# Optimization experiments

Measured on AMD Instinct MI355X. Metric: run time of the kernel, lower is better.

The kernel has to match this reference:

```python
import jax, jax.numpy as jnp
import numpy as np

HID = 128
HEADS = 4
CH = HID // HEADS          # 32
EDGE_DIM = 2 * HID         # H_update mode
GROUPS = 8
NEG_SLOPE = 0.2
EPS_GN = 1e-5
EPS_LN = 1e-5
N_NODES = 32768
N_EDGES = 524288


def setup_inputs() -> dict:
    key = jax.random.key(0)
    ks = jax.random.split(key, 32)
    N, E, C = N_NODES, N_EDGES, HID
    s = lambda fan: 1.0 / np.sqrt(fan)
    inp = dict(
        h_target=jax.random.normal(ks[0], (N, C), jnp.float32),
        h_source=jax.random.normal(ks[1], (N, C), jnp.float32),
        pos=jax.random.normal(ks[2], (N, 2), jnp.float32),
        t_emb=jax.random.normal(ks[3], (N, C), jnp.float32),
        edge_index=jax.random.randint(ks[4], (2, E), 0, N, jnp.int32),
        # AdaGN params
        gn_gamma=jnp.ones((C,), jnp.float32),
        gn_beta=jnp.zeros((C,), jnp.float32),
        fc_W=jax.random.normal(ks[5], (C, 2 * C), jnp.float32) * s(C),
        fc_b=jnp.zeros((2 * C,), jnp.float32),
        # GATv2 params
        Wl=jax.random.normal(ks[6], (C, HEADS * CH), jnp.float32) * s(C),
        bl=jnp.zeros((HEADS * CH,), jnp.float32),
        Wr=jax.random.normal(ks[7], (C, HEADS * CH), jnp.float32) * s(C),
        br=jnp.zeros((HEADS * CH,), jnp.float32),
        We=jax.random.normal(ks[8], (EDGE_DIM, HEADS * CH), jnp.float32) * s(EDGE_DIM),
        att=jax.random.normal(ks[9], (HEADS, CH), jnp.float32) * s(CH),
        gat_bias=jnp.zeros((HEADS * CH,), jnp.float32),
        # post GAT linear
        Wpost=jax.random.normal(ks[10], (C, C), jnp.float32) * s(C),
        bpost=jnp.zeros((C,), jnp.float32),
        # update MLP: LayerNorm -> Linear -> GELU -> Linear
        ln_g=jnp.ones((C,), jnp.float32),
        ln_b=jnp.zeros((C,), jnp.float32),
        W1=jax.random.normal(ks[11], (C, C), jnp.float32) * s(C),
        b1=jnp.zeros((C,), jnp.float32),
        W2=jax.random.normal(ks[12], (C, C), jnp.float32) * s(C),
        b2=jnp.zeros((C,), jnp.float32),
    )
    return inp


def _adagn(x, cond, gn_gamma, gn_beta, fc_W, fc_b):
    N, C = x.shape
    xg = x.reshape(N, GROUPS, C // GROUPS)
    mu = xg.mean(-1, keepdims=True)
    var = xg.var(-1, keepdims=True)
    normed = ((xg - mu) * jax.lax.rsqrt(var + EPS_GN)).reshape(N, C)
    normed = normed * gn_gamma + gn_beta
    style = cond @ fc_W + fc_b
    gamma, beta = jnp.split(style, 2, axis=-1)
    return normed * (1.0 + gamma) + beta


def reference(h_target, h_source, pos, t_emb, edge_index,
              gn_gamma, gn_beta, fc_W, fc_b,
              Wl, bl, Wr, br, We, att, gat_bias,
              Wpost, bpost, ln_g, ln_b, W1, b1, W2, b2):
    N, C = h_source.shape
    src, dst = edge_index[0], edge_index[1]

    h_src_mod = _adagn(h_source, t_emb, gn_gamma, gn_beta, fc_W, fc_b)

    # physics edge features (H_update mode)
    d_vec = pos[src] - pos[dst]                       # [E,2]
    dx, dy = d_vec[:, 0:1], d_vec[:, 1:2]
    dist_sq = jnp.maximum((d_vec ** 2).sum(-1, keepdims=True), 1e-8)
    grad_mag = (h_src_mod[src] - h_src_mod[dst]) / dist_sq   # [E,C]
    edge_attr = jnp.concatenate([grad_mag * (-dy), grad_mag * dx], axis=-1)  # [E,2C]

    # GATv2Conv (eval mode, no dropout)
    xl = (h_src_mod @ Wl + bl).reshape(N, HEADS, CH)  # source transform
    xr = (h_src_mod @ Wr + br).reshape(N, HEADS, CH)  # target transform
    e = (edge_attr @ We).reshape(-1, HEADS, CH)
    z = jax.nn.leaky_relu(xl[src] + xr[dst] + e, NEG_SLOPE)   # [E,H,Ch]
    logit = jnp.einsum('ehc,hc->eh', z, att)                  # [E,H]
    m = jax.ops.segment_max(logit, dst, num_segments=N)       # [N,H]
    m = jnp.where(jnp.isfinite(m), m, 0.0)
    ex = jnp.exp(logit - m[dst])
    denom = jax.ops.segment_sum(ex, dst, num_segments=N)      # [N,H]
    alpha = ex / (denom[dst] + 1e-16)                         # [E,H]
    msg = xl[src] * alpha[..., None]                          # [E,H,Ch]
    aggr = jax.ops.segment_sum(msg, dst, num_segments=N).reshape(N, HEADS * CH)
    aggr = aggr + gat_bias

    aggr = aggr @ Wpost + bpost

    # update MLP with residual
    mu = aggr.mean(-1, keepdims=True)
    var = aggr.var(-1, keepdims=True)
    ln = (aggr - mu) * jax.lax.rsqrt(var + EPS_LN) * ln_g + ln_b
    h = jax.nn.gelu(ln @ W1 + b1, approximate=False) @ W2 + b2
    return h_target + h
```

## Files before the change

### kernel.cpp

```cpp
#include <hip/hip_runtime.h>
#include <hip/hip_bf16.h>
#include <math.h>

#define HID 128

typedef __bf16 bf16x8 __attribute__((ext_vector_type(8)));
typedef float f32x4 __attribute__((ext_vector_type(4)));
typedef float nf4 __attribute__((ext_vector_type(4)));
union BF8 { uint4 u; bf16x8 v; unsigned short s[8]; };

__device__ __forceinline__ unsigned short f2bf(float x) {
  unsigned u = __float_as_uint(x);
  unsigned r = u + 0x7FFFu + ((u >> 16) & 1u);
  return (unsigned short)(r >> 16);
}
__device__ __forceinline__ float bf2f(unsigned short h) {
  return __uint_as_float(((unsigned)h) << 16);
}
__device__ __forceinline__ void ld2bf(const unsigned short* p, float& x, float& y) {
  unsigned v = *(const unsigned*)p;
  x = __uint_as_float((v & 0xFFFFu) << 16);
  y = __uint_as_float(v & 0xFFFF0000u);
}
__device__ __forceinline__ float2 pk_add2(float2 a, float2 b) {
  return make_float2(a.x + b.x, a.y + b.y);
}
__device__ __forceinline__ float2 pk_sub2(float2 a, float2 b) {
  return make_float2(a.x - b.x, a.y - b.y);
}
__device__ __forceinline__ float2 pk_fma2(float2 a, float2 b, float2 c) {
  return make_float2(fmaf(a.x, b.x, c.x), fmaf(a.y, b.y, c.y));
}
__device__ __forceinline__ float2 pk_max2(float2 a, float2 b) {
  return make_float2(fmaxf(a.x, b.x), fmaxf(a.y, b.y));
}
__device__ __forceinline__ float2 pk_muls2(float2 a, float b) {
  return make_float2(a.x * b, a.y * b);
}

__global__ __launch_bounds__(256) void k1_prep_hist(
    const float* __restrict__ fc_W, const float* __restrict__ Wl,
    const float* __restrict__ Wr, const float* __restrict__ We,
    const float* __restrict__ Wpost, const float* __restrict__ W1,
    const float* __restrict__ W2, const float* __restrict__ bl,
    const float* __restrict__ br, const float* __restrict__ gat_bias,
    const float* __restrict__ bpost,
    unsigned short* __restrict__ fcTh, unsigned short* __restrict__ fcTl,
    unsigned short* __restrict__ WnTh, unsigned short* __restrict__ WnTl,
    unsigned short* __restrict__ WpT, unsigned short* __restrict__ W1T,
    unsigned short* __restrict__ W2T,
    float* __restrict__ bxy, float* __restrict__ bpost2,
    const int* __restrict__ edst, int* __restrict__ count, int E) {
  int bid = blockIdx.x;
  if (bid >= 578) {
    int e = (bid - 578) * 256 + threadIdx.x;
    if (e < E) atomicAdd(&count[edst[e]], 1);
    return;
  }
  int gid = bid * 256 + threadIdx.x;
  if (gid < 32768) {
    int n = gid >> 7, k = gid & 127;
    float x = fc_W[k * 256 + n];
    unsigned short h = f2bf(x);
    fcTh[n * 128 + k] = h;
    fcTl[n * 128 + k] = f2bf(x - bf2f(h));
  } else if (gid < 98304) {
    int i = gid - 32768; int n = i >> 7, k = i & 127;
    float x;
    if (n < 128)      x = Wl[k * 128 + n];
    else if (n < 256) x = Wr[k * 128 + (n - 128)];
    else if (n < 384) x = We[k * 128 + (n - 256)];
    else              x = We[(128 + k) * 128 + (n - 384)];
    unsigned short h = f2bf(x);
    WnTh[n * 128 + k] = h;
    if (n >= 256) WnTl[(n - 256) * 128 + k] = f2bf(x - bf2f(h));
  } else if (gid < 147456) {
    int i = gid - 98304; int which = i >> 14; int j = i & 16383;
    int n = j >> 7, k = j & 127;
    const float* W = (which == 0) ? Wpost : (which == 1) ? W1 : W2;
    unsigned short* T = (which == 0) ? WpT : (which == 1) ? W1T : W2T;
    T[n * 128 + k] = f2bf(W[k * 128 + n]);
  } else if (gid < 147712) {
    int j = gid - 147456;
    bxy[j] = (j < 128) ? bl[j] : br[j - 128];
  } else if (gid < 147840) {
    int t = gid - 147712;
    float s = bpost[t];
    for (int k = 0; k < 128; ++k) s += gat_bias[k] * Wpost[k * 128 + t];
    bpost2[t] = s;
  }
}

__global__ __launch_bounds__(256) void k2_style_scan(
    const float* __restrict__ A, const unsigned short* __restrict__ WTh,
    const unsigned short* __restrict__ WTl, const float* __restrict__ bias,
    float* __restrict__ C,
    const int* __restrict__ count, int* __restrict__ rowptr,
    int* __restrict__ cursor, int N, int E) {
  if (blockIdx.x == 512) {
    __shared__ int wtot[4];
    int t = threadIdx.x, lane = t & 63, wv = t >> 6;
    const int4* c4 = (const int4*)count;
    int base = t * 32;
    int s = 0;
    for (int i = 0; i < 32; ++i) {
      int4 c = c4[base + i];
      s += c.x + c.y + c.z + c.w;
    }
    int incl = s;
#pragma unroll
    for (int off = 1; off < 64; off <<= 1) {
      int v = __shfl_up(incl, off);
      if (lane >= off) incl += v;
    }
    if (lane == 63) wtot[wv] = incl;
    __syncthreads();
    if (t == 0) {
      int a0 = wtot[0], a1 = wtot[1], a2 = wtot[2];
      wtot[0] = 0; wtot[1] = a0; wtot[2] = a0 + a1; wtot[3] = a0 + a1 + a2;
    }
    __syncthreads();
    int run = wtot[wv] + incl - s;
    for (int i = 0; i < 32; ++i) {
      int4 c = c4[base + i];
      int4 r;
      r.x = run; run += c.x;
      r.y = run; run += c.y;
      r.z = run; run += c.z;
      r.w = run; run += c.w;
      ((int4*)rowptr)[base + i] = r;
      ((int4*)cursor)[base + i] = r;
    }
    if (t == 255) rowptr[N] = E;
    return;
  }
  int tid = threadIdx.x;
  int wave = tid >> 6, lane = tid & 63;
  int m = lane & 15, q = lane >> 4;
  int r0 = blockIdx.x * 64 + wave * 16;
  const float* arow = A + (size_t)(r0 + m) * 128 + q * 8;
  BF8 Ah[4], Al[4];
#pragma unroll
  for (int kc = 0; kc < 4; ++kc) {
    float4 x0 = *(const float4*)(arow + kc * 32);
    float4 x1 = *(const float4*)(arow + kc * 32 + 4);
    float xs[8] = {x0.x, x0.y, x0.z, x0.w, x1.x, x1.y, x1.z, x1.w};
#pragma unroll
    for (int j = 0; j < 8; ++j) {
      unsigned short h = f2bf(xs[j]);
      Ah[kc].s[j] = h;
      Al[kc].s[j] = f2bf(xs[j] - bf2f(h));
    }
  }
  for (int nt = 0; nt < 16; ++nt) {
    const unsigned short* wr  = WTh + (size_t)(nt * 16 + m) * 128 + q * 8;
    const unsigned short* wrl = WTl + (size_t)(nt * 16 + m) * 128 + q * 8;
    f32x4 acc = {0.f, 0.f, 0.f, 0.f};
#pragma unroll
    for (int kc = 0; kc < 4; ++kc) {
      BF8 bh, blo;
      bh.u  = *(const uint4*)(wr + kc * 32);
      blo.u = *(const uint4*)(wrl + kc * 32);
      acc = __builtin_amdgcn_mfma_f32_16x16x32_bf16(Ah[kc].v, bh.v, acc, 0, 0, 0);
      acc = __builtin_amdgcn_mfma_f32_16x16x32_bf16(Al[kc].v, bh.v, acc, 0, 0, 0);
      acc = __builtin_amdgcn_mfma_f32_16x16x32_bf16(Ah[kc].v, blo.v, acc, 0, 0, 0);
    }
    int n = nt * 16 + m;
    float bv = bias[n];
#pragma unroll
    for (int i = 0; i < 4; ++i) {
      int row = r0 + q * 4 + i;
      C[(size_t)row * 256 + n] = acc[i] + bv;
    }
  }
}

__global__ __launch_bounds__(256) void k3_node_scatter(
    const float* __restrict__ h_source, const float* __restrict__ style,
    const float* __restrict__ gn_gamma, const float* __restrict__ gn_beta,
    const unsigned short* __restrict__ WnTh, const unsigned short* __restrict__ WnTl,
    const float* __restrict__ bxy,
    unsigned short* __restrict__ packed, unsigned short* __restrict__ xrArr,
    const int* __restrict__ esrc, const int* __restrict__ edst,
    const float* __restrict__ pos, int* __restrict__ cursor,
    nf4* __restrict__ meta, int E) {
  int bid = blockIdx.x;
  if (bid >= 256) {
    int e = (bid - 256) * 256 + threadIdx.x;
    if (e >= E) return;
    int src = esrc[e], dst = edst[e];
    int p = atomicAdd(&cursor[dst], 1);
    float2 ps = *(const float2*)(pos + 2 * src);
    float2 pd = *(const float2*)(pos + 2 * dst);
    float dx = ps.x - pd.x, dy = ps.y - pd.y;
    float d2 = fmaxf(dx * dx + dy * dy, 1e-8f);
    nf4 v = {__int_as_float(src), -dy / d2, dx / d2, 0.0f};
    meta[p] = v;
    return;
  }
  int tid = threadIdx.x, wave = tid >> 6, lane = tid & 63;
  int m = lane & 15, q = lane >> 4;
  int r0 = bid * 128 + wave * 32;
  BF8 Ah[2][4], Al[2][4];
#pragma unroll
  for (int set = 0; set < 2; ++set) {
    int r = r0 + set * 16 + m;
    const float* hrow = h_source + (size_t)r * 128;
    const float* srow = style + (size_t)r * 256;
#pragma unroll
    for (int kc = 0; kc < 4; ++kc) {
      int ch = q * 8 + kc * 32;
      float4 x0 = *(const float4*)(hrow + ch);
      float4 x1 = *(const float4*)(hrow + ch + 4);
      float xs[8] = {x0.x, x0.y, x0.z, x0.w, x1.x, x1.y, x1.z, x1.w};
      float s8 = 0.f, q8 = 0.f;
#pragma unroll
      for (int j = 0; j < 8; ++j) { s8 += xs[j]; q8 += xs[j] * xs[j]; }
      float s16 = s8 + __shfl_xor(s8, 16);
      float q16 = q8 + __shfl_xor(q8, 16);
      float mu = s16 * (1.0f / 16.0f);
      float var = q16 * (1.0f / 16.0f) - mu * mu;
      float rv = rsqrtf(var + 1e-5f);
      float4 g0 = *(const float4*)(gn_gamma + ch);
      float4 g1 = *(const float4*)(gn_gamma + ch + 4);
      float4 be0 = *(const float4*)(gn_beta + ch);
      float4 be1 = *(const float4*)(gn_beta + ch + 4);
      float4 sg0 = *(const float4*)(srow + ch);
      float4 sg1 = *(const float4*)(srow + ch + 4);
      float4 sb0 = *(const float4*)(srow + 128 + ch);
      float4 sb1 = *(const float4*)(srow + 128 + ch + 4);
      float gg[8] = {g0.x, g0.y, g0.z, g0.w, g1.x, g1.y, g1.z, g1.w};
      float bb[8] = {be0.x, be0.y, be0.z, be0.w, be1.x, be1.y, be1.z, be1.w};
      float sg[8] = {sg0.x, sg0.y, sg0.z, sg0.w, sg1.x, sg1.y, sg1.z, sg1.w};
      float sb[8] = {sb0.x, sb0.y, sb0.z, sb0.w, sb1.x, sb1.y, sb1.z, sb1.w};
#pragma unroll
      for (int j = 0; j < 8; ++j) {
        float v = ((xs[j] - mu) * rv * gg[j] + bb[j]) * (1.0f + sg[j]) + sb[j];
        unsigned short h = f2bf(v);
        Ah[set][kc].s[j] = h;
        Al[set][kc].s[j] = f2bf(v - bf2f(h));
      }
    }
  }
  for (int nt = 0; nt < 32; ++nt) {
    f32x4 acc0 = {0.f, 0.f, 0.f, 0.f};
    f32x4 acc1 = {0.f, 0.f, 0.f, 0.f};
    const unsigned short* wr = WnTh + (size_t)(nt * 16 + m) * 128 + q * 8;
    if (nt < 16) {
#pragma unroll
      for (int kc = 0; kc < 4; ++kc) {
        BF8 bh; bh.u = *(const uint4*)(wr + kc * 32);
        acc0 = __builtin_amdgcn_mfma_f32_16x16x32_bf16(Ah[0][kc].v, bh.v, acc0, 0, 0, 0);
        acc1 = __builtin_amdgcn_mfma_f32_16x16x32_bf16(Ah[1][kc].v, bh.v, acc1, 0, 0, 0);
      }
    } else {
      const unsigned short* wl = WnTl + (size_t)((nt - 16) * 16 + m) * 128 + q * 8;
#pragma unroll
      for (int kc = 0; kc < 4; ++kc) {
        BF8 bh, blo;
        bh.u  = *(const uint4*)(wr + kc * 32);
        blo.u = *(const uint4*)(wl + kc * 32);
        acc0 = __builtin_amdgcn_mfma_f32_16x16x32_bf16(Ah[0][kc].v, bh.v, acc0, 0, 0, 0);
        acc0 = __builtin_amdgcn_mfma_f32_16x16x32_bf16(Al[0][kc].v, bh.v, acc0, 0, 0, 0);
        acc0 = __builtin_amdgcn_mfma_f32_16x16x32_bf16(Ah[0][kc].v, blo.v, acc0, 0, 0, 0);
        acc1 = __builtin_amdgcn_mfma_f32_16x16x32_bf16(Ah[1][kc].v, bh.v, acc1, 0, 0, 0);
        acc1 = __builtin_amdgcn_mfma_f32_16x16x32_bf16(Al[1][kc].v, bh.v, acc1, 0, 0, 0);
        acc1 = __builtin_amdgcn_mfma_f32_16x16x32_bf16(Ah[1][kc].v, blo.v, acc1, 0, 0, 0);
      }
    }
    int n = nt * 16 + m;
    float bv = (nt < 16) ? bxy[n] : 0.0f;
#pragma unroll
    for (int set = 0; set < 2; ++set) {
      f32x4 a = set ? acc1 : acc0;
#pragma unroll
      for (int i = 0; i < 4; ++i) {
        int row = r0 + set * 16 + q * 4 + i;
        unsigned short h = f2bf(a[i] + bv);
        if (nt < 8)       packed[(size_t)row * 384 + n] = h;
        else if (nt < 16) xrArr[(size_t)row * 128 + (n - 128)] = h;
        else              packed[(size_t)row * 384 + 128 + (n - 256)] = h;
      }
    }
  }
}

__device__ __forceinline__ void edge_step(nf4 mt, const unsigned* __restrict__ packedW,
                                          int lane, float2 xr, float2 Ad, float2 Bd,
                                          float a0, float a1,
                                          float& m, float& l, float2& s) {
  int si = __float_as_int(mt.x);
  const unsigned* pr = packedW + (size_t)si * 192;
  unsigned wxl = pr[lane];
  unsigned wA  = pr[64 + lane];
  unsigned wB  = pr[128 + lane];
  float2 xl = make_float2(__uint_as_float(wxl << 16), __uint_as_float(wxl & 0xFFFF0000u));
  float2 A  = make_float2(__uint_as_float(wA << 16),  __uint_as_float(wA & 0xFFFF0000u));
  float2 B  = make_float2(__uint_as_float(wB << 16),  __uint_as_float(wB & 0xFFFF0000u));
  float2 z = pk_add2(xl, xr);
  z = pk_fma2(make_float2(mt.y, mt.y), pk_sub2(A, Ad), z);
  z = pk_fma2(make_float2(mt.z, mt.z), pk_sub2(B, Bd), z);
  float2 zl = pk_max2(z, pk_muls2(z, 0.2f));
  float p = fmaf(a0, zl.x, a1 * zl.y);
#pragma unroll
  for (int mm = 8; mm >= 1; mm >>= 1) p += __shfl_xor(p, mm);
  if (p <= m) {
    float ex = expf(p - m);
    l += ex;
    s = pk_fma2(make_float2(ex, ex), xl, s);
  } else {
    float sc = expf(m - p);
    l = fmaf(l, sc, 1.0f);
    s = pk_fma2(make_float2(sc, sc), s, xl);
    m = p;
  }
}

__global__ __launch_bounds__(256) void k_edge(const int* __restrict__ rowptr,
                                              const nf4* __restrict__ meta,
                                              const unsigned short* __restrict__ packed,
                                              const unsigned short* __restrict__ xrArr,
                                              const float* __restrict__ att,
                                              float* __restrict__ aggr, int N) {
  int tid = threadIdx.x;
  int d = blockIdx.x * 4 + (tid >> 6);
  if (d >= N) return;
  int lane = tid & 63;
  int c0 = lane * 2;
  float2 av = *(const float2*)(att + c0);
  const unsigned* packedW = (const unsigned*)packed;
  float2 xr, Ad, Bd;
  ld2bf(xrArr + (size_t)d * 128 + c0, xr.x, xr.y);
  {
    const unsigned* pd = packedW + (size_t)d * 192;
    unsigned wA = pd[64 + lane], wB = pd[128 + lane];
    Ad = make_float2(__uint_as_float(wA << 16), __uint_as_float(wA & 0xFFFF0000u));
    Bd = make_float2(__uint_as_float(wB << 16), __uint_as_float(wB & 0xFFFF0000u));
  }
  int beg = rowptr[d], end = rowptr[d + 1];
  float m1 = -INFINITY, l1 = 0.f; float2 s1 = make_float2(0.f, 0.f);
  float m2 = -INFINITY, l2 = 0.f; float2 s2 = make_float2(0.f, 0.f);
  int j = beg;
  if (j + 1 < end) {
    nf4 mt0 = meta[j], mt1 = meta[j + 1];
    for (; j + 3 < end; j += 2) {
      nf4 nx0 = meta[j + 2], nx1 = meta[j + 3];
      edge_step(mt0, packedW, lane, xr, Ad, Bd, av.x, av.y, m1, l1, s1);
      edge_step(mt1, packedW, lane, xr, Ad, Bd, av.x, av.y, m2, l2, s2);
      mt0 = nx0; mt1 = nx1;
    }
    edge_step(mt0, packedW, lane, xr, Ad, Bd, av.x, av.y, m1, l1, s1);
    edge_step(mt1, packedW, lane, xr, Ad, Bd, av.x, av.y, m2, l2, s2);
    j += 2;
  }
  if (j < end) {
    nf4 mt = meta[j];
    edge_step(mt, packedW, lane, xr, Ad, Bd, av.x, av.y, m1, l1, s1);
  }
  float nm = fmaxf(m1, m2);
  float sc1 = (m1 == nm) ? 1.0f : expf(m1 - nm);
  float sc2 = (m2 == nm) ? 1.0f : expf(m2 - nm);
  float l = fmaf(l1, sc1, l2 * sc2);
  float o0 = fmaf(s1.x, sc1, s2.x * sc2);
  float o1 = fmaf(s1.y, sc1, s2.y * sc2);
  float inv = 1.0f / (l + 1e-16f);
  *(float2*)&aggr[(size_t)d * 128 + c0] = make_float2(o0 * inv, o1 * inv);
}

__global__ __launch_bounds__(256) void k_mlp(const float* __restrict__ aggr,
                                             const unsigned short* __restrict__ WpT,
                                             const unsigned short* __restrict__ W1T,
                                             const unsigned short* __restrict__ W2T,
                                             const float* __restrict__ bpost2,
                                             const float* __restrict__ b1,
                                             const float* __restrict__ b2,
                                             const float* __restrict__ ln_g,
                                             const float* __restrict__ ln_b,
                                             const float* __restrict__ h_target,
                                             float* __restrict__ out) {
  __shared__ unsigned short Tb[64 * 136];
  __shared__ unsigned short Ub[64 * 136];
  int tid = threadIdx.x, wave = tid >> 6, lane = tid & 63;
  int m = lane & 15, q = lane >> 4;
  int r0 = blockIdx.x * 64 + wave * 16;
  int rb0 = wave * 16;
  BF8 Af[4];
  {
    const float* arow = aggr + (size_t)(r0 + m) * 128 + q * 8;
#pragma unroll
    for (int kc = 0; kc < 4; ++kc) {
      float4 x0 = *(const float4*)(arow + kc * 32);
      float4 x1 = *(const float4*)(arow + kc * 32 + 4);
      float xs[8] = {x0.x, x0.y, x0.z, x0.w, x1.x, x1.y, x1.z, x1.w};
#pragma unroll
      for (int jj = 0; jj < 8; ++jj) Af[kc].s[jj] = f2bf(xs[jj]);
    }
  }
  f32x4 acc[8];
#pragma unroll
  for (int t = 0; t < 8; ++t) {
    const unsigned short* wr = WpT + (size_t)(t * 16 + m) * 128 + q * 8;
    f32x4 a = {0.f, 0.f, 0.f, 0.f};
#pragma unroll
    for (int kc = 0; kc < 4; ++kc) {
      BF8 bh; bh.u = *(const uint4*)(wr + kc * 32);
      a = __builtin_amdgcn_mfma_f32_16x16x32_bf16(Af[kc].v, bh.v, a, 0, 0, 0);
    }
    acc[t] = a;
  }
  float sum[4] = {0, 0, 0, 0}, sq[4] = {0, 0, 0, 0};
#pragma unroll
  for (int t = 0; t < 8; ++t) {
    float bv = bpost2[t * 16 + m];
#pragma unroll
    for (int i = 0; i < 4; ++i) {
      float v = acc[t][i] + bv;
      acc[t][i] = v;
      sum[i] += v;
      sq[i] += v * v;
    }
  }
#pragma unroll
  for (int i = 0; i < 4; ++i) {
#pragma unroll
    for (int w = 1; w <= 8; w <<= 1) {
      sum[i] += __shfl_xor(sum[i], w);
      sq[i] += __shfl_xor(sq[i], w);
    }
  }
  float mu[4], rv[4];
#pragma unroll
  for (int i = 0; i < 4; ++i) {
    mu[i] = sum[i] * (1.0f / 128.0f);
    float var = sq[i] * (1.0f / 128.0f) - mu[i] * mu[i];
    rv[i] = rsqrtf(var + 1e-5f);
  }
#pragma unroll
  for (int t = 0; t < 8; ++t) {
    int n = t * 16 + m;
    float g = ln_g[n], b = ln_b[n];
#pragma unroll
    for (int i = 0; i < 4; ++i) {
      float v = (acc[t][i] - mu[i]) * rv[i] * g + b;
      Tb[(rb0 + q * 4 + i) * 136 + n] = f2bf(v);
    }
  }
  __syncthreads();
  BF8 Bf[4];
  {
    const unsigned short* tp = Tb + (rb0 + m) * 136 + q * 8;
#pragma unroll
    for (int kc = 0; kc < 4; ++kc) Bf[kc].u = *(const uint4*)(tp + kc * 32);
  }
#pragma unroll
  for (int t = 0; t < 8; ++t) {
    const unsigned short* wr = W1T + (size_t)(t * 16 + m) * 128 + q * 8;
    f32x4 a = {0.f, 0.f, 0.f, 0.f};
#pragma unroll
    for (int kc = 0; kc < 4; ++kc) {
      BF8 bh; bh.u = *(const uint4*)(wr + kc * 32);
      a = __builtin_amdgcn_mfma_f32_16x16x32_bf16(Bf[kc].v, bh.v, a, 0, 0, 0);
    }
    acc[t] = a;
  }
#pragma unroll
  for (int t = 0; t < 8; ++t) {
    int n = t * 16 + m;
    float bv = b1[n];
#pragma unroll
    for (int i = 0; i < 4; ++i) {
      float v = acc[t][i] + bv;
      v = 0.5f * v * (1.0f + erff(v * 0.70710678118654752f));
      Ub[(rb0 + q * 4 + i) * 136 + n] = f2bf(v);
    }
  }
  __syncthreads();
  BF8 Cf[4];
  {
    const unsigned short* up = Ub + (rb0 + m) * 136 + q * 8;
#pragma unroll
    for (int kc = 0; kc < 4; ++kc) Cf[kc].u = *(const uint4*)(up + kc * 32);
  }
#pragma unroll
  for (int t = 0; t < 8; ++t) {
    const unsigned short* wr = W2T + (size_t)(t * 16 + m) * 128 + q * 8;
    f32x4 a = {0.f, 0.f, 0.f, 0.f};
#pragma unroll
    for (int kc = 0; kc < 4; ++kc) {
      BF8 bh; bh.u = *(const uint4*)(wr + kc * 32);
      a = __builtin_amdgcn_mfma_f32_16x16x32_bf16(Cf[kc].v, bh.v, a, 0, 0, 0);
    }
    int n = t * 16 + m;
    float bv = b2[n];
#pragma unroll
    for (int i = 0; i < 4; ++i) {
      size_t off = (size_t)(r0 + q * 4 + i) * 128 + n;
      out[off] = a[i] + bv + h_target[off];
    }
  }
}

extern "C" void kernel_launch(void* const* d_in, const int* in_sizes, int n_in,
                              void* d_out, int out_size, void* d_ws, size_t ws_size,
                              hipStream_t stream) {
  const float* h_target = (const float*)d_in[0];
  const float* h_source = (const float*)d_in[1];
  const float* pos      = (const float*)d_in[2];
  const float* t_emb    = (const float*)d_in[3];
  const int*   eidx     = (const int*)d_in[4];
  const float* gn_gamma = (const float*)d_in[5];
  const float* gn_beta  = (const float*)d_in[6];
  const float* fc_W     = (const float*)d_in[7];
  const float* fc_b     = (const float*)d_in[8];
  const float* Wl       = (const float*)d_in[9];
  const float* bl       = (const float*)d_in[10];
  const float* Wr       = (const float*)d_in[11];
  const float* br       = (const float*)d_in[12];
  const float* We       = (const float*)d_in[13];
  const float* att      = (const float*)d_in[14];
  const float* gat_bias = (const float*)d_in[15];
  const float* Wpost    = (const float*)d_in[16];
  const float* bpost    = (const float*)d_in[17];
  const float* ln_g     = (const float*)d_in[18];
  const float* ln_b     = (const float*)d_in[19];
  const float* W1       = (const float*)d_in[20];
  const float* b1       = (const float*)d_in[21];
  const float* W2       = (const float*)d_in[22];
  const float* b2       = (const float*)d_in[23];

  const int N = in_sizes[0] / HID;
  const int E = in_sizes[4] / 2;
  const int* esrc = eidx;
  const int* edst = eidx + E;

  float* ws = (float*)d_ws;
  const size_t MF = 1024 * 1024;
  float* style  = ws;
  float* aggr   = ws;
  unsigned short* packed = (unsigned short*)(ws + 8 * MF);
  unsigned short* xrArr  = (unsigned short*)(ws + 14 * MF);
  nf4*   meta   = (nf4*)(ws + 16 * MF);
  int*   rowptr = (int*)(ws + 18 * MF);
  int*   count  = rowptr + 32832;
  int*   cursor = count + 32832;
  unsigned short* wgt = (unsigned short*)(ws + 18 * MF + 131072);
  unsigned short* fcTh = wgt;
  unsigned short* fcTl = wgt + 32768;
  unsigned short* WnTh = wgt + 65536;
  unsigned short* WnTl = wgt + 131072;
  unsigned short* WpT  = wgt + 163840;
  unsigned short* W1T  = wgt + 180224;
  unsigned short* W2T  = wgt + 196608;
  float* bxy    = (float*)(wgt + 212992);
  float* bpost2 = bxy + 256;
  const size_t needed = (size_t)(18 * MF + 131072 + 106496 + 512) * 4;
  if (ws_size < needed) return;

  dim3 blk(256);
  const int histB = (E + 255) / 256;

  (void)hipMemsetAsync(count, 0, (size_t)N * 4, stream);
  k1_prep_hist<<<578 + histB, blk, 0, stream>>>(
      fc_W, Wl, Wr, We, Wpost, W1, W2, bl, br, gat_bias, bpost,
      fcTh, fcTl, WnTh, WnTl, WpT, W1T, W2T, bxy, bpost2, edst, count, E);
  k2_style_scan<<<513, blk, 0, stream>>>(t_emb, fcTh, fcTl, fc_b, style,
                                         count, rowptr, cursor, N, E);
  k3_node_scatter<<<256 + histB, blk, 0, stream>>>(
      h_source, style, gn_gamma, gn_beta, WnTh, WnTl, bxy, packed, xrArr,
      esrc, edst, pos, cursor, meta, E);
  k_edge<<<(N + 3) / 4, blk, 0, stream>>>(rowptr, meta, packed, xrArr, att, aggr, N);
  k_mlp<<<N / 64, blk, 0, stream>>>(aggr, WpT, W1T, W2T, bpost2, b1, b2, ln_g, ln_b,
                                    h_target, (float*)d_out);
}
```

Measured before the change: 364.5 us.

## Interleave per-node edge features and software-pipeline gathers in the GAT edge kernel

Reorders the packed per-node buffer so each lane's xl, A and B bf16 pairs sit next to each other, so one 12-byte load per lane replaces three separate 4-byte gathers per edge. The edge loop now prefetches the gathered rows one iteration ahead to overlap gather latency with compute. It also replaces the shuffle reduction with DPP moves, uses fast __expf, and uses a lazy max-rescale threshold (+8) to skip most rescale branches. The threshold and fast exp slightly change numerics. The longer prefetch chain raises register pressure.

```diff
diff --git a/kernel.cpp b/kernel.cpp
--- a/kernel.cpp
+++ b/kernel.cpp
@@ -7,7 +7,10 @@
 typedef __bf16 bf16x8 __attribute__((ext_vector_type(8)));
 typedef float f32x4 __attribute__((ext_vector_type(4)));
 typedef float nf4 __attribute__((ext_vector_type(4)));
+typedef float v2f __attribute__((ext_vector_type(2)));
 union BF8 { uint4 u; bf16x8 v; unsigned short s[8]; };
+
+struct __attribute__((packed, aligned(4))) U3 { unsigned a, b, c; };
 
 __device__ __forceinline__ unsigned short f2bf(float x) {
   unsigned u = __float_as_uint(x);
@@ -22,20 +25,11 @@
   x = __uint_as_float((v & 0xFFFFu) << 16);
   y = __uint_as_float(v & 0xFFFF0000u);
 }
-__device__ __forceinline__ float2 pk_add2(float2 a, float2 b) {
-  return make_float2(a.x + b.x, a.y + b.y);
-}
-__device__ __forceinline__ float2 pk_sub2(float2 a, float2 b) {
-  return make_float2(a.x - b.x, a.y - b.y);
-}
-__device__ __forceinline__ float2 pk_fma2(float2 a, float2 b, float2 c) {
-  return make_float2(fmaf(a.x, b.x, c.x), fmaf(a.y, b.y, c.y));
-}
-__device__ __forceinline__ float2 pk_max2(float2 a, float2 b) {
-  return make_float2(fmaxf(a.x, b.x), fmaxf(a.y, b.y));
-}
-__device__ __forceinline__ float2 pk_muls2(float2 a, float b) {
-  return make_float2(a.x * b, a.y * b);
+__device__ __forceinline__ v2f bfpair(unsigned w) {
+  v2f r;
+  r.x = __uint_as_float(w << 16);
+  r.y = __uint_as_float(w & 0xFFFF0000u);
+  return r;
 }
 
 __global__ __launch_bounds__(256) void k1_prep_hist(
@@ -270,6 +264,16 @@
     }
     int n = nt * 16 + m;
     float bv = (nt < 16) ? bxy[n] : 0.0f;
+    int pidx;
+    if (nt < 8) {
+      pidx = 6 * (n >> 1) + (n & 1);
+    } else if (nt >= 16) {
+      int t = n - 256;
+      int c = t & 127;
+      pidx = 6 * (c >> 1) + ((t < 128) ? 2 : 4) + (c & 1);
+    } else {
+      pidx = -1;
+    }
 #pragma unroll
     for (int set = 0; set < 2; ++set) {
       f32x4 a = set ? acc1 : acc0;
@@ -277,41 +281,41 @@
       for (int i = 0; i < 4; ++i) {
         int row = r0 + set * 16 + q * 4 + i;
         unsigned short h = f2bf(a[i] + bv);
-        if (nt < 8)       packed[(size_t)row * 384 + n] = h;
-        else if (nt < 16) xrArr[(size_t)row * 128 + (n - 128)] = h;
-        else              packed[(size_t)row * 384 + 128 + (n - 256)] = h;
+        if (pidx >= 0) packed[(size_t)row * 384 + pidx] = h;
+        else           xrArr[(size_t)row * 128 + (n - 128)] = h;
       }
     }
   }
 }
 
-__device__ __forceinline__ void edge_step(nf4 mt, const unsigned* __restrict__ packedW,
-                                          int lane, float2 xr, float2 Ad, float2 Bd,
-                                          float a0, float a1,
-                                          float& m, float& l, float2& s) {
-  int si = __float_as_int(mt.x);
-  const unsigned* pr = packedW + (size_t)si * 192;
-  unsigned wxl = pr[lane];
-  unsigned wA  = pr[64 + lane];
-  unsigned wB  = pr[128 + lane];
-  float2 xl = make_float2(__uint_as_float(wxl << 16), __uint_as_float(wxl & 0xFFFF0000u));
-  float2 A  = make_float2(__uint_as_float(wA << 16),  __uint_as_float(wA & 0xFFFF0000u));
-  float2 B  = make_float2(__uint_as_float(wB << 16),  __uint_as_float(wB & 0xFFFF0000u));
-  float2 z = pk_add2(xl, xr);
-  z = pk_fma2(make_float2(mt.y, mt.y), pk_sub2(A, Ad), z);
-  z = pk_fma2(make_float2(mt.z, mt.z), pk_sub2(B, Bd), z);
-  float2 zl = pk_max2(z, pk_muls2(z, 0.2f));
-  float p = fmaf(a0, zl.x, a1 * zl.y);
-#pragma unroll
-  for (int mm = 8; mm >= 1; mm >>= 1) p += __shfl_xor(p, mm);
-  if (p <= m) {
-    float ex = expf(p - m);
+__device__ __forceinline__ float dpp_red16(float p) {
+  p += __int_as_float(__builtin_amdgcn_mov_dpp(__float_as_int(p), 0xB1, 0xF, 0xF, true));
+  p += __int_as_float(__builtin_amdgcn_mov_dpp(__float_as_int(p), 0x4E, 0xF, 0xF, true));
+  p += __int_as_float(__builtin_amdgcn_mov_dpp(__float_as_int(p), 0x141, 0xF, 0xF, true));
+  p += __int_as_float(__builtin_amdgcn_mov_dpp(__float_as_int(p), 0x140, 0xF, 0xF, true));
+  return p;
+}
+
+__device__ __forceinline__ void edge_compute(nf4 mt, U3 r, v2f xr, v2f Ad, v2f Bd,
+                                             float a0, float a1,
+                                             float& m, float& l, v2f& s) {
+  v2f xl = bfpair(r.a);
+  v2f A  = bfpair(r.b);
+  v2f B  = bfpair(r.c);
+  v2f z = xl + xr;
+  z = (A - Ad) * mt.y + z;
+  z = (B - Bd) * mt.z + z;
+  v2f zq = z * 0.2f;
+  float p = fmaf(a0, fmaxf(z.x, zq.x), a1 * fmaxf(z.y, zq.y));
+  p = dpp_red16(p);
+  if (__builtin_expect(p <= m + 8.0f, 1)) {
+    float ex = __expf(p - m);
     l += ex;
-    s = pk_fma2(make_float2(ex, ex), xl, s);
+    s = xl * ex + s;
   } else {
-    float sc = expf(m - p);
+    float sc = __expf(m - p);
     l = fmaf(l, sc, 1.0f);
-    s = pk_fma2(make_float2(sc, sc), s, xl);
+    s = s * sc + xl;
     m = p;
   }
 }
@@ -327,44 +331,67 @@
   if (d >= N) return;
   int lane = tid & 63;
   int c0 = lane * 2;
+  unsigned lane12 = (unsigned)lane * 12u;
   float2 av = *(const float2*)(att + c0);
-  const unsigned* packedW = (const unsigned*)packed;
-  float2 xr, Ad, Bd;
-  ld2bf(xrArr + (size_t)d * 128 + c0, xr.x, xr.y);
-  {
-    const unsigned* pd = packedW + (size_t)d * 192;
-    unsigned wA = pd[64 + lane], wB = pd[128 + lane];
-    Ad = make_float2(__uint_as_float(wA << 16), __uint_as_float(wA & 0xFFFF0000u));
-    Bd = make_float2(__uint_as_float(wB << 16), __uint_as_float(wB & 0xFFFF0000u));
-  }
+  const char* rbase = (const char*)packed;
+  v2f xr;
+  { float x, y; ld2bf(xrArr + (size_t)d * 128 + c0, x, y); xr.x = x; xr.y = y; }
+  U3 rd = *(const U3*)(rbase + (unsigned)d * 768u + lane12);
+  v2f Ad = bfpair(rd.b), Bd = bfpair(rd.c);
   int beg = rowptr[d], end = rowptr[d + 1];
-  float m1 = -INFINITY, l1 = 0.f; float2 s1 = make_float2(0.f, 0.f);
-  float m2 = -INFINITY, l2 = 0.f; float2 s2 = make_float2(0.f, 0.f);
-  int j = beg;
-  if (j + 1 < end) {
-    nf4 mt0 = meta[j], mt1 = meta[j + 1];
-    for (; j + 3 < end; j += 2) {
-      nf4 nx0 = meta[j + 2], nx1 = meta[j + 3];
-      edge_step(mt0, packedW, lane, xr, Ad, Bd, av.x, av.y, m1, l1, s1);
-      edge_step(mt1, packedW, lane, xr, Ad, Bd, av.x, av.y, m2, l2, s2);
-      mt0 = nx0; mt1 = nx1;
-    }
-    edge_step(mt0, packedW, lane, xr, Ad, Bd, av.x, av.y, m1, l1, s1);
-    edge_step(mt1, packedW, lane, xr, Ad, Bd, av.x, av.y, m2, l2, s2);
-    j += 2;
-  }
-  if (j < end) {
+  float m1 = -INFINITY, l1 = 0.f; v2f s1 = {0.f, 0.f};
+  float m2 = -INFINITY, l2 = 0.f; v2f s2 = {0.f, 0.f};
+  int j = beg, rem = end - beg;
+  nf4 ma0 = {}, ma1 = {}, mb0 = {}, mb1 = {};
+  U3 ra0 = {}, ra1 = {};
+  if (rem >= 2) {
+    ma0 = meta[j]; ma1 = meta[j + 1];
+    ra0 = *(const U3*)(rbase + (unsigned)__float_as_int(ma0.x) * 768u + lane12);
+    ra1 = *(const U3*)(rbase + (unsigned)__float_as_int(ma1.x) * 768u + lane12);
+    if (rem >= 4) { mb0 = meta[j + 2]; mb1 = meta[j + 3]; }
+  }
+  for (; j + 5 < end; j += 2) {
+    nf4 mc0 = meta[j + 4], mc1 = meta[j + 5];
+    U3 rb0 = *(const U3*)(rbase + (unsigned)__float_as_int(mb0.x) * 768u + lane12);
+    U3 rb1 = *(const U3*)(rbase + (unsigned)__float_as_int(mb1.x) * 768u + lane12);
+    edge_compute(ma0, ra0, xr, Ad, Bd, av.x, av.y, m1, l1, s1);
+    edge_compute(ma1, ra1, xr, Ad, Bd, av.x, av.y, m2, l2, s2);
+    ma0 = mb0; ma1 = mb1; mb0 = mc0; mb1 = mc1;
+    ra0 = rb0; ra1 = rb1;
+  }
+  rem = end - j;
+  if (rem >= 4) {
+    U3 rb0 = *(const U3*)(rbase + (unsigned)__float_as_int(mb0.x) * 768u + lane12);
+    U3 rb1 = *(const U3*)(rbase + (unsigned)__float_as_int(mb1.x) * 768u + lane12);
+    edge_compute(ma0, ra0, xr, Ad, Bd, av.x, av.y, m1, l1, s1);
+    edge_compute(ma1, ra1, xr, Ad, Bd, av.x, av.y, m2, l2, s2);
+    edge_compute(mb0, rb0, xr, Ad, Bd, av.x, av.y, m1, l1, s1);
+    edge_compute(mb1, rb1, xr, Ad, Bd, av.x, av.y, m2, l2, s2);
+    if (rem == 5) {
+      nf4 mt = meta[j + 4];
+      U3 r = *(const U3*)(rbase + (unsigned)__float_as_int(mt.x) * 768u + lane12);
+      edge_compute(mt, r, xr, Ad, Bd, av.x, av.y, m1, l1, s1);
+    }
+  } else if (rem >= 2) {
+    edge_compute(ma0, ra0, xr, Ad, Bd, av.x, av.y, m1, l1, s1);
+    edge_compute(ma1, ra1, xr, Ad, Bd, av.x, av.y, m2, l2, s2);
+    if (rem == 3) {
+      nf4 mt = meta[j + 2];
+      U3 r = *(const U3*)(rbase + (unsigned)__float_as_int(mt.x) * 768u + lane12);
+      edge_compute(mt, r, xr, Ad, Bd, av.x, av.y, m1, l1, s1);
+    }
+  } else if (rem == 1) {
     nf4 mt = meta[j];
-    edge_step(mt, packedW, lane, xr, Ad, Bd, av.x, av.y, m1, l1, s1);
+    U3 r = *(const U3*)(rbase + (unsigned)__float_as_int(mt.x) * 768u + lane12);
+    edge_compute(mt, r, xr, Ad, Bd, av.x, av.y, m1, l1, s1);
   }
   float nm = fmaxf(m1, m2);
-  float sc1 = (m1 == nm) ? 1.0f : expf(m1 - nm);
-  float sc2 = (m2 == nm) ? 1.0f : expf(m2 - nm);
+  float sc1 = (m1 == nm) ? 1.0f : __expf(m1 - nm);
+  float sc2 = (m2 == nm) ? 1.0f : __expf(m2 - nm);
   float l = fmaf(l1, sc1, l2 * sc2);
-  float o0 = fmaf(s1.x, sc1, s2.x * sc2);
-  float o1 = fmaf(s1.y, sc1, s2.y * sc2);
+  v2f o = s1 * sc1 + s2 * sc2;
   float inv = 1.0f / (l + 1e-16f);
-  *(float2*)&aggr[(size_t)d * 128 + c0] = make_float2(o0 * inv, o1 * inv);
+  *(float2*)&aggr[(size_t)d * 128 + c0] = make_float2(o.x * inv, o.y * inv);
 }
 
 __global__ __launch_bounds__(256) void k_mlp(const float* __restrict__ aggr,
```

New measurement: 358.1 us. About the same (-1.8%).
